# Kernel tuning notes

Measured on AMD Instinct MI355X. Metric: run time of the kernel, lower is better.

## Reference

```python
import jax, jax.numpy as jnp
import numpy as np

N, E, D_IN, D_OUT, H = 50000, 800000, 128, 128, 4
D_H = D_OUT // H


def setup_inputs() -> dict:
    key = jax.random.key(0)
    ks = jax.random.split(key, 6)
    x = jax.random.normal(ks[0], (N, D_IN), dtype=jnp.float32)
    edge_index = jax.random.randint(ks[1], (2, E), 0, N, dtype=jnp.int64)
    # parameters (xavier-ish scaling)
    W = jax.random.normal(ks[2], (D_IN, D_OUT), dtype=jnp.float32) * (1.0 / np.sqrt(D_IN))
    attn_vec = jax.random.normal(ks[3], (H, 2 * D_H), dtype=jnp.float32) * (1.0 / np.sqrt(2 * D_H))
    out_w = jax.random.normal(ks[4], (D_OUT, D_OUT), dtype=jnp.float32) * (1.0 / np.sqrt(D_OUT))
    out_b = jax.random.normal(ks[5], (D_OUT,), dtype=jnp.float32) * 0.01
    return {"x": x, "edge_index": edge_index, "W": W, "attn_vec": attn_vec,
            "out_w": out_w, "out_b": out_b}


def reference(x, edge_index, W, attn_vec, out_w, out_b):
    n = x.shape[0]
    Wx = (x @ W).reshape(n, H, D_H)                      # [N,H,d_h]
    src, dst = edge_index[0], edge_index[1]
    h_src = Wx[src]                                      # [E,H,d_h]
    h_dst = Wx[dst]                                      # [E,H,d_h]
    a_i = attn_vec[:, :D_H]                              # [H,d_h]
    a_j = attn_vec[:, D_H:]                              # [H,d_h]
    e = jnp.einsum('ehd,hd->eh', h_src, a_i) + jnp.einsum('ehd,hd->eh', h_dst, a_j)
    e = jax.nn.leaky_relu(e, negative_slope=0.2)         # [E,H]
    # segment softmax over incoming edges per destination node
    e_max = jax.ops.segment_max(e, dst, num_segments=n)  # [N,H]
    exp_e = jnp.exp(e - e_max[dst])                      # [E,H]
    exp_sum = jax.ops.segment_sum(exp_e, dst, num_segments=n)  # [N,H]
    alpha = exp_e / (exp_sum[dst] + 1e-16)               # [E,H]
    # weighted scatter-add aggregation
    agg = jax.ops.segment_sum(alpha[:, :, None] * h_src, dst, num_segments=n)  # [N,H,d_h]
    out = agg.reshape(n, D_OUT) @ out_w + out_b
    return jax.nn.elu(out)
```

## Files before the change

### kernel.cpp

```cpp
#include <hip/hip_runtime.h>
#include <math.h>


typedef __attribute__((ext_vector_type(8))) short short8;
typedef __attribute__((ext_vector_type(4))) float f32x4;

#define BIN_VPT 16

__device__ __forceinline__ float lrelu(float v) { return v >= 0.f ? v : 0.2f * v; }

__device__ __forceinline__ unsigned short f2bf(float f) {
  unsigned int u = __float_as_uint(f);
  u += 0x7FFFu + ((u >> 16) & 1u);
  return (unsigned short)(u >> 16);
}
__device__ __forceinline__ unsigned int cvt_pk_bf16(float lo, float hi) {
  unsigned int r;
  asm("v_cvt_pk_bf16_f32 %0, %1, %2" : "=v"(r) : "v"(lo), "v"(hi));
  return r;
}
__device__ __forceinline__ float bflo(unsigned int w) { return __uint_as_float(w << 16); }
__device__ __forceinline__ float bfhi(unsigned int w) { return __uint_as_float(w & 0xFFFF0000u); }

__device__ __forceinline__ int blk_excl_scan(int v, int* ws) {
  const int t = threadIdx.x, lane = t & 63, wv = t >> 6;
  int incl = v;
#pragma unroll
  for (int m = 1; m < 64; m <<= 1) {
    int x = __shfl_up(incl, m, 64);
    if (lane >= m) incl += x;
  }
  if (lane == 63) ws[wv] = incl;
  __syncthreads();
  int woff = 0;
  for (int p = 0; p < wv; ++p) woff += ws[p];
  return woff + incl - v;
}

__global__ void k_setup(const float* __restrict__ W, const float* __restrict__ ow,
                        unsigned short* __restrict__ wf, unsigned short* __restrict__ owf,
                        int* __restrict__ gcnt, int* __restrict__ gcur) {
  const int t = blockIdx.x * 256 + threadIdx.x;
  if (blockIdx.x == 0) gcnt[threadIdx.x] = 0;
  if (blockIdx.x == 1) gcur[threadIdx.x] = 0;
  const int which = t >> 11;
  const int tt = t & 2047;
  const float* M = which ? ow : W;
  unsigned short* F = which ? owf : wf;
  const int lane = tt & 63;
  const int nt = (tt >> 6) & 7;
  const int ks = tt >> 9;
  const int k0 = ks * 32 + (lane >> 4) * 8;
  const int col = nt * 16 + (lane & 15);
  short8 v;
#pragma unroll
  for (int j = 0; j < 8; ++j) v[j] = (short)f2bf(M[(k0 + j) * 128 + col]);
  *(short8*)(F + (size_t)tt * 8) = v;
}

__global__ void k_gemm1b(const float* __restrict__ x, const unsigned short* __restrict__ wf,
                         const float* __restrict__ attn, unsigned int* __restrict__ Wxb,
                         float* __restrict__ s_i, float* __restrict__ s_j, int n,
                         const int* __restrict__ dst, int* __restrict__ gcnt, int E,
                         int gemmBlocks) {
  __shared__ int lc[256];
  if (blockIdx.x >= gemmBlocks) {
    const int bb = blockIdx.x - gemmBlocks;
    lc[threadIdx.x] = 0;
    __syncthreads();
    const int base = bb * (256 * BIN_VPT);
#pragma unroll
    for (int j = 0; j < BIN_VPT; ++j) {
      int e = base + j * 256 + threadIdx.x;
      if (e < E) atomicAdd(&lc[((unsigned int)dst[e]) >> 8], 1);
    }
    __syncthreads();
    int c = lc[threadIdx.x];
    if (c) atomicAdd(&gcnt[threadIdx.x], c);
    return;
  }

  const int lane = threadIdx.x & 63;
  const int gw = blockIdx.x * (blockDim.x >> 6) + (threadIdx.x >> 6);
  const int r0 = gw * 16;
  if (r0 >= n) return;
  const int g = lane >> 4, c = lane & 15;

  f32x4 acc[8];
#pragma unroll
  for (int nt = 0; nt < 8; ++nt) acc[nt] = (f32x4){0.f, 0.f, 0.f, 0.f};

  const int arow = min(r0 + c, n - 1);
#pragma unroll
  for (int ks = 0; ks < 4; ++ks) {
    const float* xr = x + (size_t)arow * 128 + ks * 32 + g * 8;
    float4 v0 = *(const float4*)xr;
    float4 v1 = *(const float4*)(xr + 4);
    uint4 au;
    au.x = cvt_pk_bf16(v0.x, v0.y);
    au.y = cvt_pk_bf16(v0.z, v0.w);
    au.z = cvt_pk_bf16(v1.x, v1.y);
    au.w = cvt_pk_bf16(v1.z, v1.w);
    short8 af = __builtin_bit_cast(short8, au);
#pragma unroll
    for (int nt = 0; nt < 8; ++nt) {
      short8 bf = *(const short8*)(wf + ((size_t)(ks * 8 + nt) * 64 + lane) * 8);
      acc[nt] = __builtin_amdgcn_mfma_f32_16x16x32_bf16(af, bf, acc[nt], 0, 0, 0);
    }
  }

  const int odd = c & 1;
#pragma unroll
  for (int r = 0; r < 4; ++r) {
    const int row = r0 + g * 4 + r;
    if (row >= n) continue;
    unsigned int* dp = Wxb + (size_t)row * 64;
#pragma unroll
    for (int ntp = 0; ntp < 4; ++ntp) {
      float ve = acc[ntp][r], vo = acc[ntp + 4][r];
      float vex = __shfl_xor(ve, 1, 64);
      float vox = __shfl_xor(vo, 1, 64);
      const int nt = odd ? ntp + 4 : ntp;
      dp[nt * 8 + (c >> 1)] = cvt_pk_bf16(odd ? vox : ve, odd ? vo : vex);
    }
  }

  float aiv[8], ajv[8];
#pragma unroll
  for (int nt = 0; nt < 8; ++nt) {
    const int hh = nt >> 1, ch = (nt & 1) * 16 + c;
    aiv[nt] = attn[hh * 64 + ch];
    ajv[nt] = attn[hh * 64 + 32 + ch];
  }
#pragma unroll
  for (int r = 0; r < 4; ++r) {
    float pih[4], pjh[4];
#pragma unroll
    for (int h = 0; h < 4; ++h) {
      pih[h] = acc[2 * h][r] * aiv[2 * h] + acc[2 * h + 1][r] * aiv[2 * h + 1];
      pjh[h] = acc[2 * h][r] * ajv[2 * h] + acc[2 * h + 1][r] * ajv[2 * h + 1];
    }
#pragma unroll
    for (int m = 1; m < 16; m <<= 1) {
#pragma unroll
      for (int h = 0; h < 4; ++h) {
        pih[h] += __shfl_xor(pih[h], m, 64);
        pjh[h] += __shfl_xor(pjh[h], m, 64);
      }
    }
    const int row = r0 + g * 4 + r;
    if (c == 0 && row < n) {
#pragma unroll
      for (int h = 0; h < 4; ++h) {
        s_i[(size_t)row * 4 + h] = pih[h];
        s_j[(size_t)row * 4 + h] = pjh[h];
      }
    }
  }
}

__global__ void k_bin1(const int* __restrict__ edges, const int* __restrict__ gcnt,
                       int* __restrict__ gcur, unsigned int* __restrict__ tmp, int E) {
  __shared__ int ws[4];
  __shared__ int bst_s[256];
  __shared__ int lcnt[256];
  __shared__ int lbase[256];
  const int t = threadIdx.x;
  const int excl = blk_excl_scan(gcnt[t], ws);
  bst_s[t] = excl;
  lcnt[t] = 0;
  __syncthreads();
  const int base = blockIdx.x * (256 * BIN_VPT);
  unsigned int pv[BIN_VPT];
  int rk[BIN_VPT];
#pragma unroll
  for (int j = 0; j < BIN_VPT; ++j) {
    int e = base + j * 256 + t;
    if (e < E) {
      unsigned int s = (unsigned int)edges[e];
      unsigned int d = (unsigned int)edges[E + e];
      pv[j] = s | (d << 16);
      rk[j] = atomicAdd(&lcnt[d >> 8], 1);
    } else {
      pv[j] = 0u;
      rk[j] = -1;
    }
  }
  __syncthreads();
  const int c = lcnt[t];
  lbase[t] = bst_s[t] + (c ? atomicAdd(&gcur[t], c) : 0);
  __syncthreads();
#pragma unroll
  for (int j = 0; j < BIN_VPT; ++j) {
    if (rk[j] >= 0) {
      const int b = pv[j] >> 24;
      tmp[lbase[b] + rk[j]] = pv[j];
    }
  }
}

__global__ void k_bin2(const unsigned int* __restrict__ tmp, const int* __restrict__ gcnt,
                       const float* __restrict__ s_i, const float* __restrict__ s_j,
                       int* __restrict__ csr, float* __restrict__ pexp,
                       int* __restrict__ offs, int* __restrict__ cnts, int n) {
  __shared__ int ws[4];
  __shared__ int bst_s[256];
  __shared__ int nc[256];
  __shared__ float sjs[256][4];
  const int b = blockIdx.x;
  const int t = threadIdx.x;
  bst_s[t] = blk_excl_scan(gcnt[t], ws);
  nc[t] = 0;
  {
    const int node = b * 256 + t;
    float4 sj = make_float4(0.f, 0.f, 0.f, 0.f);
    if (node < n) sj = *(const float4*)(s_j + (size_t)node * 4);
    *(float4*)&sjs[t][0] = sj;
  }
  __syncthreads();
  const int base = bst_s[b], cnt = gcnt[b];
  for (int i = t; i < cnt; i += 256)
    atomicAdd(&nc[(tmp[base + i] >> 16) & 255], 1);
  __syncthreads();
  const int node = b * 256 + t;
  const int c = nc[t];
  if (node < n) cnts[node] = c;
  __syncthreads();
  const int excl = blk_excl_scan(c, ws);
  if (node < n) offs[node] = base + excl;
  __syncthreads();
  nc[t] = excl;
  __syncthreads();
  for (int i = t; i < cnt; i += 256) {
    unsigned int v = tmp[base + i];
    const int srcv = (int)(v & 0xFFFFu);
    const int loc = (v >> 16) & 255;
    int pos = atomicAdd(&nc[loc], 1);
    const float4 si = *(const float4*)(s_i + (size_t)srcv * 4);
    const float4 sj = *(const float4*)&sjs[loc][0];
    float4 p;
    p.x = __expf(lrelu(si.x + sj.x));
    p.y = __expf(lrelu(si.y + sj.y));
    p.z = __expf(lrelu(si.z + sj.z));
    p.w = __expf(lrelu(si.w + sj.w));
    csr[base + pos] = srcv;
    *(float4*)(pexp + (size_t)(base + pos) * 4) = p;
  }
}

#define AGG_EDGE(e)                                                     \
  {                                                                     \
    int s_ = lsrc[wv][e];                                               \
    float p_ = lp[wv][e][h];                                            \
    unsigned int w_ = Wxb[(unsigned)(s_ << 6) | (unsigned)lane];        \
    acc.x += p_ * bflo(w_);                                             \
    acc.y += p_ * bfhi(w_);                                             \
    smh += p_;                                                          \
  }

__global__ void k_aggm(const unsigned int* __restrict__ Wxb,
                       const int* __restrict__ offs, const int* __restrict__ cnts,
                       const int* __restrict__ csr_src, const float* __restrict__ pexp,
                       const unsigned short* __restrict__ owf, const float* __restrict__ ob,
                       float* __restrict__ out, int n) {
  __shared__ unsigned int aTile[16][65];
  __shared__ int   lsrc[4][64];
  __shared__ float lp[4][64][4];
  const int lane = threadIdx.x & 63;
  const int wv = threadIdx.x >> 6;
  const int nd0 = blockIdx.x * 16;
  const int nd0w = nd0 + wv * 4;
  const int h = lane >> 4;

  int degv = 0;
  if (lane < 4 && nd0w + lane < n) degv = cnts[nd0w + lane];
  const int wbase = (nd0w < n) ? offs[nd0w] : 0;
  const int d0 = __shfl(degv, 0, 64), d1 = __shfl(degv, 1, 64);
  const int d2 = __shfl(degv, 2, 64), d3 = __shfl(degv, 3, 64);
  const int b0 = d0, b1 = d0 + d1, b2 = b1 + d2;
  const int tot = b2 + d3;

  int cur = 0;
  int rem = d0;
  float2 acc = make_float2(0.f, 0.f);
  float smh = 0.f;

  while (cur < 4 && rem == 0) {
    if (nd0w + cur < n) aTile[(wv << 2) + cur][lane] = 0u;
    ++cur;
    rem = (cur == 1) ? d1 : (cur == 2) ? d2 : (cur == 3) ? d3 : 0;
  }

  for (int c0 = 0; c0 < tot; c0 += 64) {
    const int m = min(64, tot - c0);
    if (lane < m) {
      lsrc[wv][lane] = csr_src[wbase + c0 + lane];
      *(float4*)&lp[wv][lane][0] = *(const float4*)(pexp + (size_t)(wbase + c0 + lane) * 4);
    }
    asm volatile("s_waitcnt lgkmcnt(0)" ::: "memory");
    int k = 0;
    while (k < m) {
      const int take = min(m - k, rem);
      int e = k;
      const int end = k + take;
      for (; e + 8 <= end; e += 8) {
        AGG_EDGE(e + 0) AGG_EDGE(e + 1) AGG_EDGE(e + 2) AGG_EDGE(e + 3)
        AGG_EDGE(e + 4) AGG_EDGE(e + 5) AGG_EDGE(e + 6) AGG_EDGE(e + 7)
      }
      for (; e + 4 <= end; e += 4) {
        AGG_EDGE(e + 0) AGG_EDGE(e + 1) AGG_EDGE(e + 2) AGG_EDGE(e + 3)
      }
      for (; e < end; ++e) AGG_EDGE(e)
      k += take;
      rem -= take;
      while (rem == 0 && cur < 4) {
        const float inv = 1.f / (smh + 1e-16f);
        if (nd0w + cur < n)
          aTile[(wv << 2) + cur][lane] = cvt_pk_bf16(acc.x * inv, acc.y * inv);
        ++cur;
        acc.x = 0.f; acc.y = 0.f; smh = 0.f;
        rem = (cur == 1) ? d1 : (cur == 2) ? d2 : (cur == 3) ? d3 : 0;
      }
      if (cur >= 4) break;
    }
  }
  __syncthreads();

  const int g = lane >> 4, c = lane & 15;
#pragma unroll
  for (int t2 = 0; t2 < 2; ++t2) {
    const int nt = wv + t2 * 4;
    f32x4 o = (f32x4){0.f, 0.f, 0.f, 0.f};
#pragma unroll
    for (int ks = 0; ks < 4; ++ks) {
      uint4 au = *(const uint4*)&aTile[c][ks * 16 + g * 4];
      short8 af = __builtin_bit_cast(short8, au);
      short8 bf = *(const short8*)(owf + ((size_t)(ks * 8 + nt) * 64 + lane) * 8);
      o = __builtin_amdgcn_mfma_f32_16x16x32_bf16(af, bf, o, 0, 0, 0);
    }
#pragma unroll
    for (int r = 0; r < 4; ++r) {
      const int row = nd0 + g * 4 + r;
      if (row < n) {
        float v = o[r] + ob[nt * 16 + c];
        v = v > 0.f ? v : expm1f(v);
        out[(size_t)row * 128 + nt * 16 + c] = v;
      }
    }
  }
}

extern "C" void kernel_launch(void* const* d_in, const int* in_sizes, int n_in,
                              void* d_out, int out_size, void* d_ws, size_t ws_size,
                              hipStream_t stream) {
  const float* x    = (const float*)d_in[0];
  const int*   edges = (const int*)d_in[1];
  const float* W    = (const float*)d_in[2];
  const float* attn = (const float*)d_in[3];
  const float* ow   = (const float*)d_in[4];
  const float* ob   = (const float*)d_in[5];
  const int n = in_sizes[0] / 128;
  const int E = in_sizes[1] / 2;
  float* out = (float*)d_out;

  char* wp = (char*)d_ws;
  auto alloc = [&](size_t bytes) {
    char* p = wp;
    wp += (bytes + 255) & ~(size_t)255;
    return p;
  };
  unsigned short* wf  = (unsigned short*)alloc(2048 * 8 * 2);
  unsigned short* owf = (unsigned short*)alloc(2048 * 8 * 2);
  unsigned int*   Wxb = (unsigned int*)alloc((size_t)n * 64 * 4);
  float* s_i    = (float*)alloc((size_t)n * 4 * 4);
  float* s_j    = (float*)alloc((size_t)n * 4 * 4);
  int*   gcnt   = (int*)alloc(256 * 4);
  int*   gcur   = (int*)alloc(256 * 4);
  int*   offs   = (int*)alloc((size_t)n * 4);
  int*   cnts   = (int*)alloc((size_t)n * 4);
  unsigned int* tmp = (unsigned int*)alloc((size_t)E * 4);
  int*   csr    = (int*)alloc((size_t)E * 4);
  float* pexp   = (float*)alloc((size_t)E * 4 * 4);

  dim3 blk(256);
  const int NB = (n + 255) / 256;
  const int EB = (E + 256 * BIN_VPT - 1) / (256 * BIN_VPT);
  const int strips = (n + 15) / 16;
  const int gemmBlocks = (strips + 3) / 4;

  k_setup<<<16, blk, 0, stream>>>(W, ow, wf, owf, gcnt, gcur);
  k_gemm1b<<<gemmBlocks + EB, blk, 0, stream>>>(x, wf, attn, Wxb, s_i, s_j, n,
                                                edges + E, gcnt, E, gemmBlocks);
  k_bin1<<<EB, blk, 0, stream>>>(edges, gcnt, gcur, tmp, E);
  k_bin2<<<NB, blk, 0, stream>>>(tmp, gcnt, s_i, s_j, csr, pexp, offs, cnts, n);
  k_aggm<<<(n + 15) / 16, blk, 0, stream>>>(Wxb, offs, cnts, csr, pexp,
                                            owf, ob, out, n);
}
```

Measured before the change: 102.4 us.

## Split Wx into per-column-block slabs and aggregate per slab, separate output GEMM

Wx is now stored column-blocked (8 slabs of 16 columns per node) and the exp-scores are stored head-major. The aggregation kernel is split across 8 slab blocks per node group, so each slab (n*32 bytes) is small enough to stay cache-resident during random gathers. Each 8-lane group handles one edge, and partial sums are reduced with shuffles. The output projection moves to a separate GEMM kernel that runs in place on the fp32 aggregate. The cost is an extra launch, an fp32 round trip through the output buffer, and the csr indices and scores being reread once per slab.

```diff
diff --git a/kernel.cpp b/kernel.cpp
--- a/kernel.cpp
+++ b/kernel.cpp
@@ -59,7 +59,7 @@
 }
 
 __global__ void k_gemm1b(const float* __restrict__ x, const unsigned short* __restrict__ wf,
-                         const float* __restrict__ attn, unsigned int* __restrict__ Wxb,
+                         const float* __restrict__ attn, unsigned int* __restrict__ WxbB,
                          float* __restrict__ s_i, float* __restrict__ s_j, int n,
                          const int* __restrict__ dst, int* __restrict__ gcnt, int E,
                          int gemmBlocks) {
@@ -114,14 +114,14 @@
   for (int r = 0; r < 4; ++r) {
     const int row = r0 + g * 4 + r;
     if (row >= n) continue;
-    unsigned int* dp = Wxb + (size_t)row * 64;
 #pragma unroll
     for (int ntp = 0; ntp < 4; ++ntp) {
       float ve = acc[ntp][r], vo = acc[ntp + 4][r];
       float vex = __shfl_xor(ve, 1, 64);
       float vox = __shfl_xor(vo, 1, 64);
       const int nt = odd ? ntp + 4 : ntp;
-      dp[nt * 8 + (c >> 1)] = cvt_pk_bf16(odd ? vox : ve, odd ? vo : vex);
+      WxbB[((size_t)nt * n + row) * 8 + (c >> 1)] =
+          cvt_pk_bf16(odd ? vox : ve, odd ? vo : vex);
     }
   }
 
@@ -202,7 +202,7 @@
 __global__ void k_bin2(const unsigned int* __restrict__ tmp, const int* __restrict__ gcnt,
                        const float* __restrict__ s_i, const float* __restrict__ s_j,
                        int* __restrict__ csr, float* __restrict__ pexp,
-                       int* __restrict__ offs, int* __restrict__ cnts, int n) {
+                       int* __restrict__ offs, int* __restrict__ cnts, int n, int E) {
   __shared__ int ws[4];
   __shared__ int bst_s[256];
   __shared__ int nc[256];
@@ -235,117 +235,114 @@
     unsigned int v = tmp[base + i];
     const int srcv = (int)(v & 0xFFFFu);
     const int loc = (v >> 16) & 255;
-    int pos = atomicAdd(&nc[loc], 1);
+    int pos = base + atomicAdd(&nc[loc], 1);
     const float4 si = *(const float4*)(s_i + (size_t)srcv * 4);
     const float4 sj = *(const float4*)&sjs[loc][0];
-    float4 p;
-    p.x = __expf(lrelu(si.x + sj.x));
-    p.y = __expf(lrelu(si.y + sj.y));
-    p.z = __expf(lrelu(si.z + sj.z));
-    p.w = __expf(lrelu(si.w + sj.w));
-    csr[base + pos] = srcv;
-    *(float4*)(pexp + (size_t)(base + pos) * 4) = p;
-  }
-}
-
-#define AGG_EDGE(e)                                                     \
-  {                                                                     \
-    int s_ = lsrc[wv][e];                                               \
-    float p_ = lp[wv][e][h];                                            \
-    unsigned int w_ = Wxb[(unsigned)(s_ << 6) | (unsigned)lane];        \
-    acc.x += p_ * bflo(w_);                                             \
-    acc.y += p_ * bfhi(w_);                                             \
-    smh += p_;                                                          \
-  }
-
-__global__ void k_aggm(const unsigned int* __restrict__ Wxb,
+    csr[pos] = srcv;
+    pexp[0 * (size_t)E + pos] = __expf(lrelu(si.x + sj.x));
+    pexp[1 * (size_t)E + pos] = __expf(lrelu(si.y + sj.y));
+    pexp[2 * (size_t)E + pos] = __expf(lrelu(si.z + sj.z));
+    pexp[3 * (size_t)E + pos] = __expf(lrelu(si.w + sj.w));
+  }
+}
+
+#define AGGC_FULL(kk)                                                     \
+  {                                                                       \
+    const int pos_ = base + (kk) + eg;                                    \
+    const int src_ = csr[pos_];                                           \
+    const float p_ = pe[pos_];                                            \
+    const unsigned int w_ = slab[((size_t)src_ << 3) | (unsigned)cl];     \
+    a0 += p_ * bflo(w_); a1 += p_ * bfhi(w_); smh += p_;                  \
+  }
+#define AGGC_TAIL(kk)                                                     \
+  {                                                                       \
+    const int c1_ = deg - (kk);                                           \
+    const int pos_ = base + (kk) + min(eg, c1_ - 1);                      \
+    const int src_ = csr[pos_];                                           \
+    const float p_ = (eg < c1_) ? pe[pos_] : 0.f;                         \
+    const unsigned int w_ = slab[((size_t)src_ << 3) | (unsigned)cl];     \
+    a0 += p_ * bflo(w_); a1 += p_ * bfhi(w_); smh += p_;                  \
+  }
+
+__global__ void k_aggc(const unsigned int* __restrict__ WxbB,
                        const int* __restrict__ offs, const int* __restrict__ cnts,
-                       const int* __restrict__ csr_src, const float* __restrict__ pexp,
-                       const unsigned short* __restrict__ owf, const float* __restrict__ ob,
-                       float* __restrict__ out, int n) {
-  __shared__ unsigned int aTile[16][65];
-  __shared__ int   lsrc[4][64];
-  __shared__ float lp[4][64][4];
+                       const int* __restrict__ csr, const float* __restrict__ pexp,
+                       float* __restrict__ out, int n, int E) {
+  const int b = blockIdx.x & 7;
+  const int ng = blockIdx.x >> 3;
   const int lane = threadIdx.x & 63;
   const int wv = threadIdx.x >> 6;
-  const int nd0 = blockIdx.x * 16;
-  const int nd0w = nd0 + wv * 4;
-  const int h = lane >> 4;
-
-  int degv = 0;
-  if (lane < 4 && nd0w + lane < n) degv = cnts[nd0w + lane];
-  const int wbase = (nd0w < n) ? offs[nd0w] : 0;
-  const int d0 = __shfl(degv, 0, 64), d1 = __shfl(degv, 1, 64);
-  const int d2 = __shfl(degv, 2, 64), d3 = __shfl(degv, 3, 64);
-  const int b0 = d0, b1 = d0 + d1, b2 = b1 + d2;
-  const int tot = b2 + d3;
-
-  int cur = 0;
-  int rem = d0;
-  float2 acc = make_float2(0.f, 0.f);
-  float smh = 0.f;
-
-  while (cur < 4 && rem == 0) {
-    if (nd0w + cur < n) aTile[(wv << 2) + cur][lane] = 0u;
-    ++cur;
-    rem = (cur == 1) ? d1 : (cur == 2) ? d2 : (cur == 3) ? d3 : 0;
-  }
-
-  for (int c0 = 0; c0 < tot; c0 += 64) {
-    const int m = min(64, tot - c0);
-    if (lane < m) {
-      lsrc[wv][lane] = csr_src[wbase + c0 + lane];
-      *(float4*)&lp[wv][lane][0] = *(const float4*)(pexp + (size_t)(wbase + c0 + lane) * 4);
-    }
-    asm volatile("s_waitcnt lgkmcnt(0)" ::: "memory");
+  const int eg = lane >> 3;
+  const int cl = lane & 7;
+  const unsigned int* slab = WxbB + (size_t)b * n * 8;
+  const float* pe = pexp + (size_t)(b >> 1) * E;
+  const int nd0w = ng * 16 + wv * 4;
+
+#pragma unroll
+  for (int cur = 0; cur < 4; ++cur) {
+    const int node = nd0w + cur;
+    if (node >= n) break;
+    const int base = offs[node];
+    const int deg = cnts[node];
+    float a0 = 0.f, a1 = 0.f, smh = 0.f;
     int k = 0;
-    while (k < m) {
-      const int take = min(m - k, rem);
-      int e = k;
-      const int end = k + take;
-      for (; e + 8 <= end; e += 8) {
-        AGG_EDGE(e + 0) AGG_EDGE(e + 1) AGG_EDGE(e + 2) AGG_EDGE(e + 3)
-        AGG_EDGE(e + 4) AGG_EDGE(e + 5) AGG_EDGE(e + 6) AGG_EDGE(e + 7)
-      }
-      for (; e + 4 <= end; e += 4) {
-        AGG_EDGE(e + 0) AGG_EDGE(e + 1) AGG_EDGE(e + 2) AGG_EDGE(e + 3)
-      }
-      for (; e < end; ++e) AGG_EDGE(e)
-      k += take;
-      rem -= take;
-      while (rem == 0 && cur < 4) {
-        const float inv = 1.f / (smh + 1e-16f);
-        if (nd0w + cur < n)
-          aTile[(wv << 2) + cur][lane] = cvt_pk_bf16(acc.x * inv, acc.y * inv);
-        ++cur;
-        acc.x = 0.f; acc.y = 0.f; smh = 0.f;
-        rem = (cur == 1) ? d1 : (cur == 2) ? d2 : (cur == 3) ? d3 : 0;
-      }
-      if (cur >= 4) break;
-    }
-  }
-  __syncthreads();
-
+    for (; k + 16 <= deg; k += 16) { AGGC_FULL(k) AGGC_FULL(k + 8) }
+    if (k + 8 <= deg) { AGGC_FULL(k) k += 8; }
+    if (k < deg) AGGC_TAIL(k)
+#pragma unroll
+    for (int mm = 8; mm < 64; mm <<= 1) {
+      a0 += __shfl_xor(a0, mm, 64);
+      a1 += __shfl_xor(a1, mm, 64);
+      smh += __shfl_xor(smh, mm, 64);
+    }
+    const float inv = 1.f / (smh + 1e-16f);
+    if (eg == 0)
+      *(float2*)(out + (size_t)node * 128 + b * 16 + cl * 2) =
+          make_float2(a0 * inv, a1 * inv);
+  }
+}
+
+__global__ void k_gemm2(float* __restrict__ io, const unsigned short* __restrict__ owf,
+                        const float* __restrict__ ob, int n) {
+  const int lane = threadIdx.x & 63;
+  const int gw = blockIdx.x * (blockDim.x >> 6) + (threadIdx.x >> 6);
+  const int r0 = gw * 16;
+  if (r0 >= n) return;
   const int g = lane >> 4, c = lane & 15;
-#pragma unroll
-  for (int t2 = 0; t2 < 2; ++t2) {
-    const int nt = wv + t2 * 4;
-    f32x4 o = (f32x4){0.f, 0.f, 0.f, 0.f};
-#pragma unroll
-    for (int ks = 0; ks < 4; ++ks) {
-      uint4 au = *(const uint4*)&aTile[c][ks * 16 + g * 4];
-      short8 af = __builtin_bit_cast(short8, au);
+
+  f32x4 acc[8];
+#pragma unroll
+  for (int nt = 0; nt < 8; ++nt) acc[nt] = (f32x4){0.f, 0.f, 0.f, 0.f};
+
+  const int arow = min(r0 + c, n - 1);
+#pragma unroll
+  for (int ks = 0; ks < 4; ++ks) {
+    const float* xr = io + (size_t)arow * 128 + ks * 32 + g * 8;
+    float4 v0 = *(const float4*)xr;
+    float4 v1 = *(const float4*)(xr + 4);
+    uint4 au;
+    au.x = cvt_pk_bf16(v0.x, v0.y);
+    au.y = cvt_pk_bf16(v0.z, v0.w);
+    au.z = cvt_pk_bf16(v1.x, v1.y);
+    au.w = cvt_pk_bf16(v1.z, v1.w);
+    short8 af = __builtin_bit_cast(short8, au);
+#pragma unroll
+    for (int nt = 0; nt < 8; ++nt) {
       short8 bf = *(const short8*)(owf + ((size_t)(ks * 8 + nt) * 64 + lane) * 8);
-      o = __builtin_amdgcn_mfma_f32_16x16x32_bf16(af, bf, o, 0, 0, 0);
-    }
-#pragma unroll
-    for (int r = 0; r < 4; ++r) {
-      const int row = nd0 + g * 4 + r;
-      if (row < n) {
-        float v = o[r] + ob[nt * 16 + c];
-        v = v > 0.f ? v : expm1f(v);
-        out[(size_t)row * 128 + nt * 16 + c] = v;
-      }
+      acc[nt] = __builtin_amdgcn_mfma_f32_16x16x32_bf16(af, bf, acc[nt], 0, 0, 0);
+    }
+  }
+
+#pragma unroll
+  for (int r = 0; r < 4; ++r) {
+    const int row = r0 + g * 4 + r;
+    if (row >= n) continue;
+    float* dst = io + (size_t)row * 128;
+#pragma unroll
+    for (int nt = 0; nt < 8; ++nt) {
+      float v = acc[nt][r] + ob[nt * 16 + c];
+      v = v > 0.f ? v : expm1f(v);
+      dst[nt * 16 + c] = v;
     }
   }
 }
@@ -371,7 +368,7 @@
   };
   unsigned short* wf  = (unsigned short*)alloc(2048 * 8 * 2);
   unsigned short* owf = (unsigned short*)alloc(2048 * 8 * 2);
-  unsigned int*   Wxb = (unsigned int*)alloc((size_t)n * 64 * 4);
+  unsigned int*   WxbB = (unsigned int*)alloc((size_t)n * 64 * 4);
   float* s_i    = (float*)alloc((size_t)n * 4 * 4);
   float* s_j    = (float*)alloc((size_t)n * 4 * 4);
   int*   gcnt   = (int*)alloc(256 * 4);
@@ -387,12 +384,13 @@
   const int EB = (E + 256 * BIN_VPT - 1) / (256 * BIN_VPT);
   const int strips = (n + 15) / 16;
   const int gemmBlocks = (strips + 3) / 4;
+  const int aggBlocks = 8 * ((n + 15) / 16);
 
   k_setup<<<16, blk, 0, stream>>>(W, ow, wf, owf, gcnt, gcur);
-  k_gemm1b<<<gemmBlocks + EB, blk, 0, stream>>>(x, wf, attn, Wxb, s_i, s_j, n,
+  k_gemm1b<<<gemmBlocks + EB, blk, 0, stream>>>(x, wf, attn, WxbB, s_i, s_j, n,
                                                 edges + E, gcnt, E, gemmBlocks);
   k_bin1<<<EB, blk, 0, stream>>>(edges, gcnt, gcur, tmp, E);
-  k_bin2<<<NB, blk, 0, stream>>>(tmp, gcnt, s_i, s_j, csr, pexp, offs, cnts, n);
-  k_aggm<<<(n + 15) / 16, blk, 0, stream>>>(Wxb, offs, cnts, csr, pexp,
-                                            owf, ob, out, n);
-}
+  k_bin2<<<NB, blk, 0, stream>>>(tmp, gcnt, s_i, s_j, csr, pexp, offs, cnts, n, E);
+  k_aggc<<<aggBlocks, blk, 0, stream>>>(WxbB, offs, cnts, csr, pexp, out, n, E);
+  k_gemm2<<<gemmBlocks, blk, 0, stream>>>(out, owf, ob, n);
+}
```

Result: slower. 173.5 us (+69.5%).
